# Kernel optimization log

Measured on AMD Instinct MI355X. Metric: run time of the kernel, lower is better.

The kernel has to match this reference:

```python
import jax, jax.numpy as jnp
import numpy as np

EPS = 1e-6


def _feature_map(x):
    # elu(x) + 1
    return jax.nn.elu(x) + 1.0


def _causal_dot(Qb, Kb, V):
    """Causal linear attention numerator for 3 stacked branches.
    Qb, Kb: [3, N, L, H, D]; V: [N, L, H, Dv] -> out [3, N, L, H, Dv].
    out[b,n,l,h,:] = sum_{s<=l} (Qb[b,n,l,h,:] . Kb[b,n,s,h,:]) V[n,s,h,:]
    computed with an O(L) recurrent scan over cumulative KV outer products.
    """
    Qs = jnp.moveaxis(Qb, 2, 0)  # [L, 3, N, H, D]
    Ks = jnp.moveaxis(Kb, 2, 0)  # [L, 3, N, H, D]
    Vs = jnp.moveaxis(V, 1, 0)   # [L, N, H, Dv]
    B, N, _, H, D = Qb.shape
    Dv = V.shape[-1]
    S0 = jnp.zeros((B, N, H, D, Dv), dtype=Qb.dtype)

    def step(S, inp):
        q, k, v = inp  # q,k: [3,N,H,D], v: [N,H,Dv]
        S = S + k[..., :, None] * v[None, :, :, None, :]
        o = jnp.einsum('bnhi,bnhij->bnhj', q, S)
        return S, o

    _, out = jax.lax.scan(step, S0, (Qs, Ks, Vs))  # out: [L,3,N,H,Dv]
    return jnp.moveaxis(out, 0, 2)  # [3,N,L,H,Dv]


def setup_inputs() -> dict:
    key = jax.random.key(0)
    ks = jax.random.split(key, 5)
    N, L, H, D = 4, 2048, 8, 128
    return {
        'queries': jax.random.normal(ks[0], (N, L, H, D), dtype=jnp.float32),
        'q2': jax.random.normal(ks[1], (N, L, H, D), dtype=jnp.float32),
        'keys': jax.random.normal(ks[2], (N, L, H, D), dtype=jnp.float32),
        'values': jax.random.normal(ks[3], (N, L, H, D), dtype=jnp.float32),
        'key_lengths': jnp.ones((N, L), dtype=jnp.float32),
        'omega': jax.random.normal(ks[4], (H, D, D), dtype=jnp.float32),
    }


def reference(queries, q2, keys, values, key_lengths, omega):
    N, L, H, D = queries.shape
    Q = _feature_map(queries)                       # [N,L,H,D]
    K = _feature_map(keys) * key_lengths[:, :, None, None]

    # Delta[n,l,h,i] = l/L for all n,h,i -> projection through omega reduces to
    # (l/L) * sum_i omega[h,i,j], same math as einsum('nlhi,hij->nlhj', Delta, omega).
    delta = (jnp.arange(L, dtype=queries.dtype) / L)        # [L]
    t = delta[:, None, None] * jnp.sum(omega, axis=1)[None]  # [L,H,D]
    sin_t, cos_t = jnp.sin(t), jnp.cos(t)
    s2, c2, sc = sin_t ** 2, cos_t ** 2, sin_t * cos_t       # [L,H,D] each

    # Q_term = sin(phi(q2))^2 * feature_map(queries)
    q2_proj = jnp.einsum('nlhi,hij->nlhj', q2, omega)
    Q_term = (jnp.sin(q2_proj) ** 2) * Q                     # [N,L,H,D]

    # Branch trig weights: Q gets [sin^2, cos^2, sin*cos], K gets [cos^2, sin^2, sin*cos]
    wq = jnp.stack([s2, c2, sc])[:, None]  # [3,1,L,H,D]
    wk = jnp.stack([c2, s2, sc])[:, None]
    Qb = Q_term[None] * wq                 # [3,N,L,H,D]
    Kb = K[None] * wk                      # [3,N,L,H,D]

    # Denominator terms Z_b = <Q_b[l], cumsum_{s<=l} K_b[s]>
    Kcum = jnp.cumsum(Kb, axis=2)
    Z = jnp.einsum('bnlhi,bnlhi->bnlh', Qb, Kcum)   # [3,N,L,H]

    Vb = _causal_dot(Qb, Kb, values)                # [3,N,L,H,D]

    numerator = Vb[0] + Vb[1] - 2.0 * Vb[2]
    denominator = Z[0] + Z[1] - 2.0 * Z[2] + EPS
    return numerator / denominator[:, :, :, None]
```

## Files before the change

kernel.cpp:

```cpp
#include <hip/hip_runtime.h>


typedef float f32x4 __attribute__((ext_vector_type(4)));
typedef short s16x8 __attribute__((ext_vector_type(8)));
typedef short s16x4 __attribute__((ext_vector_type(4)));
typedef unsigned short u16;

static constexpr int    Ln   = 2048;
static constexpr size_t NHLD = (size_t)32 * 2048 * 128;
static constexpr size_t KSB  = (size_t)32 * 16 * 128;

__device__ __forceinline__ float b2f(u16 s) {
  union { unsigned u; float f; } x; x.u = ((unsigned)s) << 16; return x.f;
}
__device__ __forceinline__ u16 f2b(float f) {
  union { float f; unsigned u; } x; x.f = f;
  unsigned r = x.u + 0x7fffu + ((x.u >> 16) & 1u);
  return (u16)(r >> 16);
}
__device__ __forceinline__ s16x8 pack8(f32x4 a, f32x4 b) {
  s16x8 r;
  r[0] = (short)f2b(a[0]); r[1] = (short)f2b(a[1]); r[2] = (short)f2b(a[2]); r[3] = (short)f2b(a[3]);
  r[4] = (short)f2b(b[0]); r[5] = (short)f2b(b[1]); r[6] = (short)f2b(b[2]); r[7] = (short)f2b(b[3]);
  return r;
}

__global__ __launch_bounds__(256) void k_omega(const float* __restrict__ om,
                                               u16* __restrict__ wt, float* __restrict__ osum) {
  __shared__ alignas(16) u16 T[128][136];
  int h = blockIdx.x, t = threadIdx.x;
  for (int idx = t; idx < 128 * 32; idx += 256) {
    int i = idx >> 5, cs = (idx & 31) << 2;
    f32x4 vv = *(const f32x4*)(om + ((size_t)(h * 128 + i)) * 128 + cs);
    T[i][cs + 0] = f2b(vv[0]); T[i][cs + 1] = f2b(vv[1]);
    T[i][cs + 2] = f2b(vv[2]); T[i][cs + 3] = f2b(vv[3]);
  }
  if (t < 128) {
    float acc = 0.f;
    for (int i = 0; i < 128; i++) acc += om[((size_t)(h * 128 + i)) * 128 + t];
    osum[h * 128 + t] = acc;
  }
  __syncthreads();
  {
    int j = t >> 1, lh = (t & 1) << 6;
    s16x8* dst = (s16x8*)(wt + ((size_t)(h * 128 + j)) * 128 + lh);
    for (int u = 0; u < 8; u++) {
      s16x8 pv;
#pragma unroll
      for (int e = 0; e < 8; e++) pv[e] = (short)T[lh + u * 8 + e][j];
      dst[u] = pv;
    }
  }
}

__global__ __launch_bounds__(256) void k_kvfeat(const float* __restrict__ kg, const float* __restrict__ vg,
                                                const float* __restrict__ klg, const float* __restrict__ osum,
                                                u16* __restrict__ kb3, u16* __restrict__ vt) {
  __shared__ alignas(16) u16 T[128][128];
  int bid = blockIdx.x, t = threadIdx.x;
  int c = bid & 15, h = (bid >> 4) & 7, n = bid >> 7;
  int l0 = c << 7, nh = (n << 3) + h;
  const float invL = 1.0f / 2048.0f;
  int gcol = t & 31, cs = gcol << 2;
  f32x4 osv = *(const f32x4*)(osum + h * 128 + cs);
#pragma unroll
  for (int it = 0; it < 16; it++) {
    int idx = (it << 8) + t;
    int rr = idx >> 5;
    int l = l0 + rr;
    size_t gb = (((size_t)(n * Ln + l) * 8 + h) << 7) + cs;
    f32x4 kv = *(const f32x4*)(kg + gb);
    f32x4 vv = *(const f32x4*)(vg + gb);
    float klv = klg[n * Ln + l];
    float tb = (float)l * invL;
    u16 r0[4], r1[4], r2[4];
#pragma unroll
    for (int e = 0; e < 4; e++) {
      float kf = (kv[e] > 0.f ? kv[e] + 1.f : __expf(kv[e])) * klv;
      float tt = tb * osv[e];
      float s, cc; __sincosf(tt, &s, &cc);
      r0[e] = f2b(kf * cc * cc);
      r1[e] = f2b(kf * s * s);
      r2[e] = f2b(kf * s * cc);
    }
    int gs = (gcol ^ (rr >> 3)) << 2;
    *(s16x4*)&T[rr][gs] = (s16x4){(short)f2b(vv[0]), (short)f2b(vv[1]),
                                  (short)f2b(vv[2]), (short)f2b(vv[3])};
    size_t nb = ((size_t)nh * Ln + l) * 128 + cs;
    *(s16x4*)(kb3 + nb)          = (s16x4){(short)r0[0], (short)r0[1], (short)r0[2], (short)r0[3]};
    *(s16x4*)(kb3 + NHLD + nb)   = (s16x4){(short)r1[0], (short)r1[1], (short)r1[2], (short)r1[3]};
    *(s16x4*)(kb3 + 2*NHLD + nb) = (s16x4){(short)r2[0], (short)r2[1], (short)r2[2], (short)r2[3]};
  }
  __syncthreads();
  {
    size_t bv = ((size_t)(nh * 16 + c)) << 14;
    for (int idx = t; idx < 2048; idx += 256) {
      int i = idx >> 4, o = idx & 15;
      int gp = (((i >> 2) ^ o) << 2) + (i & 3);
      s16x8 v1;
#pragma unroll
      for (int u = 0; u < 8; u++) v1[u] = (short)T[(o << 3) + u][gp];
      *(s16x8*)(vt + bv + (((size_t)i) << 7) + (o << 3)) = v1;
    }
  }
}

__global__ __launch_bounds__(512, 4) void p1a(const u16* __restrict__ vtg, const u16* __restrict__ kb3,
                                              u16* __restrict__ sct, float* __restrict__ ksum) {
  __shared__ alignas(16) u16 B[128][136];
  int bid = blockIdx.x, t = threadIdx.x;
  int c = bid & 15, h = (bid >> 4) & 7, n = (bid >> 7) & 3, b = bid >> 9;
  int l0 = c << 7, nh = (n << 3) + h, bnh = b * 32 + nh;
  int lane = t & 63, quad = lane >> 4, nl = lane & 15, w = t >> 6;
  const u16* kb = kb3 + (size_t)b * NHLD + ((size_t)nh * Ln + l0) * 128;
  for (int idx = t; idx < 2048; idx += 512) {
    int s = idx >> 4, io = idx & 15;
    s16x8 v = *(const s16x8*)(kb + (((size_t)s) << 7) + (io << 3));
    int cp = s ^ ((io & 7) << 3);
#pragma unroll
    for (int j = 0; j < 8; j++) B[(io << 3) + j][cp] = (u16)(short)v[j];
  }
  __syncthreads();
  f32x4 z4 = {0.f, 0.f, 0.f, 0.f};
  f32x4 acc[8];
#pragma unroll
  for (int i = 0; i < 8; i++) acc[i] = z4;
  int arow = (w << 4) + nl;
  size_t vbase = ((size_t)(nh * 16 + c)) << 14;
  for (int ks = 0; ks < 4; ks++) {
    int k0 = (ks << 5) + (quad << 3);
#pragma unroll
    for (int ct = 0; ct < 8; ct++) {
      int r = (ct << 4) + nl;
      int koff = k0 ^ (((r >> 3) & 7) << 3);
      s16x8 bv = *(const s16x8*)&B[r][koff];
      s16x8 av = *(const s16x8*)(vtg + vbase + (((size_t)arow) << 7) + k0);
      acc[ct] = __builtin_amdgcn_mfma_f32_16x16x32_bf16(av, bv, acc[ct], 0, 0, 0);
    }
  }
  if (t < 128) {
    float s = 0.f;
    int sw = ((t >> 3) & 7) << 3;
#pragma unroll 4
    for (int g = 0; g < 128; g += 8) {
      s16x8 v = *(const s16x8*)&B[t][g ^ sw];
#pragma unroll
      for (int e = 0; e < 8; e++) s += b2f((u16)v[e]);
    }
    ksum[(size_t)(bnh * 16 + c) * 128 + t] = s;
  }
  __syncthreads();
  {
    int lbase = (w << 4) + (quad << 2);
#pragma unroll
    for (int ct = 0; ct < 8; ct++) {
      int i = (ct << 4) + nl;
#pragma unroll
      for (int r = 0; r < 4; r++) B[lbase + r][i] = f2b(acc[ct][r]);
    }
  }
  __syncthreads();
  size_t sbase = ((size_t)(bnh * 16 + c)) << 14;
  for (int idx = t; idx < 2048; idx += 512) {
    int jr = idx >> 4, g = (idx & 15) << 3;
    *(s16x8*)(sct + sbase + ((size_t)jr << 7) + g) = *(const s16x8*)&B[jr][g];
  }
}

__global__ __launch_bounds__(256) void p1b(u16* __restrict__ sct, float* __restrict__ ksum) {
  int bid = blockIdx.x, t = threadIdx.x;
  if (bid < 768) {
    int tid = bid * 256 + t;
    int bnh = tid >> 11, rem = tid & 2047;
    size_t base = ((size_t)bnh << 18) + ((size_t)rem << 3);
    float acc[8] = {0.f, 0.f, 0.f, 0.f, 0.f, 0.f, 0.f, 0.f};
    for (int c = 0; c < 16; c++) {
      size_t a = base + ((size_t)c << 14);
      s16x8 v = *(const s16x8*)(sct + a);
      s16x8 o;
#pragma unroll
      for (int e = 0; e < 8; e++) { o[e] = (short)f2b(acc[e]); acc[e] += b2f((u16)v[e]); }
      *(s16x8*)(sct + a) = o;
    }
  } else {
    int m2 = (bid - 768) * 256 + t;
    int i = m2 & 127, bnh = m2 >> 7;
    size_t base = (size_t)bnh * 2048 + i;
    float acc = 0.f;
    for (int c = 0; c < 16; c++) {
      size_t a = base + (size_t)c * 128;
      float v = ksum[a];
      ksum[a] = acc;
      acc += v;
    }
  }
}

__global__ __launch_bounds__(256, 2) void k_qfeat(const float* __restrict__ q2g, const float* __restrict__ qg,
                                                  const u16* __restrict__ wt, const float* __restrict__ osum,
                                                  const float* __restrict__ kspre,
                                                  u16* __restrict__ qb3, float* __restrict__ zintg) {
  __shared__ alignas(16) u16 B[128][136];
  __shared__ float osb[128];
  int bid = blockIdx.x, t = threadIdx.x;
  int m = bid & 31, h = (bid >> 5) & 7, n = bid >> 8;
  int l0 = m << 6, c = m >> 1, nh = (n << 3) + h;
  if (t < 128) osb[t] = osum[h * 128 + t];
  for (int idx = t; idx < 2048; idx += 256) {
    int j = idx >> 4, cs = (idx & 15) << 3;
    *(s16x8*)&B[j][cs] = *(const s16x8*)(wt + ((size_t)(h * 128 + j)) * 128 + cs);
  }
  __syncthreads();
  int lane = t & 63, quad = lane >> 4, nl = lane & 15, w = t >> 6;
  f32x4 z4 = {0.f, 0.f, 0.f, 0.f};
  f32x4 acc[8];
#pragma unroll
  for (int i = 0; i < 8; i++) acc[i] = z4;
  int arow = l0 + (w << 4) + nl;
  for (int ks = 0; ks < 4; ks++) {
    int k0 = (ks << 5) + (quad << 3);
    const float* ap = q2g + (((size_t)(n * Ln + arow) * 8 + h) << 7) + k0;
    s16x8 av = pack8(*(const f32x4*)ap, *(const f32x4*)(ap + 4));
#pragma unroll
    for (int ct = 0; ct < 8; ct++) {
      s16x8 bv = *(const s16x8*)&B[(ct << 4) + nl][k0];
      acc[ct] = __builtin_amdgcn_mfma_f32_16x16x32_bf16(av, bv, acc[ct], 0, 0, 0);
    }
  }
  __syncthreads();
  {
    int lbase = (w << 4) + (quad << 2);
#pragma unroll
    for (int ct = 0; ct < 8; ct++) {
      int j = (ct << 4) + nl;
#pragma unroll
      for (int r = 0; r < 4; r++) {
        float sp = __sinf(acc[ct][r]);
        B[lbase + r][j] = f2b(sp * sp);
      }
    }
  }
  __syncthreads();
  const float invL = 1.0f / 2048.0f;
  for (int idx = t; idx < 1024; idx += 256) {
    int l = idx >> 4, j0 = (idx & 15) << 3, gl = l0 + l;
    s16x8 s2v = *(const s16x8*)&B[l][j0];
    const float* qp = qg + (((size_t)(n * Ln + gl) * 8 + h) << 7) + j0;
    f32x4 qa = *(const f32x4*)qp, qbv = *(const f32x4*)(qp + 4);
    size_t kbb = ((size_t)nh * 16 + c) * 128 + j0;
    f32x4 kp0a = *(const f32x4*)(kspre + kbb),           kp0b = *(const f32x4*)(kspre + kbb + 4);
    f32x4 kp1a = *(const f32x4*)(kspre + kbb + KSB),     kp1b = *(const f32x4*)(kspre + kbb + KSB + 4);
    f32x4 kp2a = *(const f32x4*)(kspre + kbb + 2 * KSB), kp2b = *(const f32x4*)(kspre + kbb + 2 * KSB + 4);
    s16x8 o0, o1, o2;
    float z = 0.f;
    float tb = (float)gl * invL;
#pragma unroll
    for (int e = 0; e < 8; e++) {
      float s2p = b2f((u16)s2v[e]);
      float qv = (e < 4) ? qa[e] : qbv[e - 4];
      float f = qv > 0.f ? qv + 1.f : __expf(qv);
      float Qt = s2p * f;
      float tt = tb * osb[j0 + e];
      float s, cc; __sincosf(tt, &s, &cc);
      float v0 = Qt * s * s, v1 = Qt * cc * cc, v2 = -2.f * Qt * s * cc;
      float k0v = (e < 4) ? kp0a[e] : kp0b[e - 4];
      float k1v = (e < 4) ? kp1a[e] : kp1b[e - 4];
      float k2v = (e < 4) ? kp2a[e] : kp2b[e - 4];
      z += v0 * k0v + v1 * k1v + v2 * k2v;
      o0[e] = (short)f2b(v0); o1[e] = (short)f2b(v1); o2[e] = (short)f2b(v2);
    }
    size_t base = ((size_t)nh * Ln + gl) * 128 + j0;
    *(s16x8*)(qb3 + base)            = o0;
    *(s16x8*)(qb3 + base + NHLD)     = o1;
    *(s16x8*)(qb3 + base + 2 * NHLD) = o2;
    z += __shfl_xor(z, 1); z += __shfl_xor(z, 2);
    z += __shfl_xor(z, 4); z += __shfl_xor(z, 8);
    if (nl == 0) zintg[(size_t)nh * Ln + gl] = z;
  }
}

__global__ __launch_bounds__(512, 4) void p3(const u16* __restrict__ qb3, const u16* __restrict__ kb3,
                                             const u16* __restrict__ vtg, const u16* __restrict__ sct,
                                             const float* __restrict__ zintg, float* __restrict__ outg) {
  __shared__ union {
    struct { alignas(16) u16 T0[128][128]; alignas(16) u16 T1[128][128]; } s;
    alignas(16) float O[128][132];
  } sm;
  int bid = blockIdx.x, t = threadIdx.x;
  int c = bid & 15, h = (bid >> 4) & 7, n = bid >> 7;
  int l0c = c << 7, nh = (n << 3) + h;
  int lane = t & 63, quad = lane >> 4, nl = lane & 15, w = t >> 6;
  f32x4 z4 = {0.f, 0.f, 0.f, 0.f};
  f32x4 accP[8], accO[8];
#pragma unroll
  for (int i = 0; i < 8; i++) { accP[i] = z4; accO[i] = z4; }
  int arow = l0c + (w << 4) + nl;
  for (int b = 0; b < 3; b++) {
    int bnh = b * 32 + nh;
    __syncthreads();
    for (int idx = t; idx < 2048; idx += 512) {
      int s = idx >> 4;
      int co = (((idx & 15) ^ (s & 7)) << 3);
      *(s16x8*)&sm.s.T0[s][co] = *(const s16x8*)(kb3 + (((size_t)bnh * Ln + l0c + s) << 7) + ((idx & 15) << 3));
    }
    size_t sbase = ((size_t)(bnh * 16 + c)) << 14;
    for (int idx = t; idx < 2048; idx += 512) {
      int j = idx >> 4;
      int co = (((idx & 15) ^ (j & 7)) << 3);
      *(s16x8*)&sm.s.T1[j][co] = *(const s16x8*)(sct + sbase + ((size_t)j << 7) + ((idx & 15) << 3));
    }
    s16x8 av[4];
#pragma unroll
    for (int ks = 0; ks < 4; ks++)
      av[ks] = *(const s16x8*)(qb3 + (((size_t)bnh * Ln + arow) << 7) + (ks << 5) + (quad << 3));
    __syncthreads();
    for (int ks = 0; ks < 4; ks++) {
      int k0 = (ks << 5) + (quad << 3);
#pragma unroll
      for (int ct = 0; ct < 8; ct++) {
        int r = (ct << 4) + nl;
        int koff = k0 ^ ((r & 7) << 3);
        s16x8 bv0 = *(const s16x8*)&sm.s.T0[r][koff];
        accP[ct] = __builtin_amdgcn_mfma_f32_16x16x32_bf16(av[ks], bv0, accP[ct], 0, 0, 0);
        s16x8 bv1 = *(const s16x8*)&sm.s.T1[r][koff];
        accO[ct] = __builtin_amdgcn_mfma_f32_16x16x32_bf16(av[ks], bv1, accO[ct], 0, 0, 0);
      }
    }
  }
  __syncthreads();
  float zP[4] = {0.f, 0.f, 0.f, 0.f};
  int lbase = (w << 4) + (quad << 2);
#pragma unroll
  for (int ct = 0; ct < 8; ct++) {
    int ss = (ct << 4) + nl;
#pragma unroll
    for (int r = 0; r < 4; r++) {
      int lr = lbase + r;
      float pv = (ss <= lr) ? accP[ct][r] : 0.f;
      zP[r] += pv;
      sm.s.T0[lr][ss ^ ((lr & 7) << 3)] = f2b(pv);
    }
  }
#pragma unroll
  for (int mteam = 1; mteam <= 8; mteam <<= 1) {
#pragma unroll
    for (int r = 0; r < 4; r++) zP[r] += __shfl_xor(zP[r], mteam);
  }
  size_t vbase = ((size_t)(nh * 16 + c)) << 14;
  for (int idx = t; idx < 2048; idx += 512) {
    int j = idx >> 4;
    int co = (((idx & 15) ^ (j & 7)) << 3);
    *(s16x8*)&sm.s.T1[j][co] = *(const s16x8*)(vtg + vbase + ((size_t)idx << 3));
  }
  float zf[4];
#pragma unroll
  for (int r = 0; r < 4; r++)
    zf[r] = zintg[(size_t)nh * Ln + l0c + lbase + r] + zP[r] + 1e-6f;
  __syncthreads();
  for (int ks = 0; ks < 4; ks++) {
    int k0 = (ks << 5) + (quad << 3);
    int rw = (w << 4) + nl;
    s16x8 pav = *(const s16x8*)&sm.s.T0[rw][k0 ^ ((rw & 7) << 3)];
#pragma unroll
    for (int ct = 0; ct < 8; ct++) {
      int r = (ct << 4) + nl;
      s16x8 vv = *(const s16x8*)&sm.s.T1[r][k0 ^ ((r & 7) << 3)];
      accO[ct] = __builtin_amdgcn_mfma_f32_16x16x32_bf16(pav, vv, accO[ct], 0, 0, 0);
    }
  }
  __syncthreads();
#pragma unroll
  for (int ct = 0; ct < 8; ct++) {
    int j = (ct << 4) + nl;
#pragma unroll
    for (int r = 0; r < 4; r++) sm.O[lbase + r][j] = accO[ct][r] / zf[r];
  }
  __syncthreads();
  for (int idx = t; idx < 4096; idx += 512) {
    int l = idx >> 5, g = (idx & 31) << 2;
    *(f32x4*)(outg + (((size_t)(n * Ln + l0c + l) * 8 + h) << 7) + g) = *(const f32x4*)&sm.O[l][g];
  }
}

extern "C" void kernel_launch(void* const* d_in, const int* in_sizes, int n_in,
                              void* d_out, int out_size, void* d_ws, size_t ws_size,
                              hipStream_t stream) {
  (void)in_sizes; (void)n_in; (void)out_size; (void)ws_size;
  const float* q   = (const float*)d_in[0];
  const float* q2  = (const float*)d_in[1];
  const float* kk  = (const float*)d_in[2];
  const float* vv  = (const float*)d_in[3];
  const float* kl  = (const float*)d_in[4];
  const float* om  = (const float*)d_in[5];
  float* out = (float*)d_out;

  u16* W     = (u16*)d_ws;
  u16* qb3   = W;
  u16* kb3   = W + 3 * NHLD;
  u16* vt    = W + 6 * NHLD;
  u16* sct   = W + 7 * NHLD;
  u16* wt    = W + 10 * NHLD;
  float* ks  = (float*)(W + 10 * NHLD + 131072);
  float* osm = ks + 196608;
  float* zin = osm + 1024;

  k_omega <<<8,    256, 0, stream>>>(om, wt, osm);
  k_kvfeat<<<512,  256, 0, stream>>>(kk, vv, kl, osm, kb3, vt);
  p1a     <<<1536, 512, 0, stream>>>(vt, kb3, sct, ks);
  p1b     <<<816,  256, 0, stream>>>(sct, ks);
  k_qfeat <<<1024, 256, 0, stream>>>(q2, q, wt, osm, ks, qb3, zin);
  p3      <<<512,  512, 0, stream>>>(qb3, kb3, vt, sct, zin, out);
}
```

Measured before the change: 270.2 us.

## Fuse K/V feature kernel with per-chunk KV outer-product kernel

Result: no change. 269.2 us (-0.4%).

```diff
diff --git a/kernel.cpp b/kernel.cpp
--- a/kernel.cpp
+++ b/kernel.cpp
@@ -53,10 +53,14 @@
   }
 }
 
-__global__ __launch_bounds__(256) void k_kvfeat(const float* __restrict__ kg, const float* __restrict__ vg,
-                                                const float* __restrict__ klg, const float* __restrict__ osum,
-                                                u16* __restrict__ kb3, u16* __restrict__ vt) {
-  __shared__ alignas(16) u16 T[128][128];
+__global__ __launch_bounds__(512) void k_kvs(const float* __restrict__ kg, const float* __restrict__ vg,
+                                             const float* __restrict__ klg, const float* __restrict__ osum,
+                                             u16* __restrict__ kb3, u16* __restrict__ vt,
+                                             u16* __restrict__ sct, float* __restrict__ ksum) {
+  __shared__ union {
+    alignas(16) u16 VT[128][128];
+    alignas(16) u16 KT[128][136];
+  } sm;
   int bid = blockIdx.x, t = threadIdx.x;
   int c = bid & 15, h = (bid >> 4) & 7, n = bid >> 7;
   int l0 = c << 7, nh = (n << 3) + h;
@@ -64,9 +68,8 @@
   int gcol = t & 31, cs = gcol << 2;
   f32x4 osv = *(const f32x4*)(osum + h * 128 + cs);
 #pragma unroll
-  for (int it = 0; it < 16; it++) {
-    int idx = (it << 8) + t;
-    int rr = idx >> 5;
+  for (int it = 0; it < 8; it++) {
+    int rr = (it << 4) + (t >> 5);
     int l = l0 + rr;
     size_t gb = (((size_t)(n * Ln + l) * 8 + h) << 7) + cs;
     f32x4 kv = *(const f32x4*)(kg + gb);
@@ -84,86 +87,80 @@
       r2[e] = f2b(kf * s * cc);
     }
     int gs = (gcol ^ (rr >> 3)) << 2;
-    *(s16x4*)&T[rr][gs] = (s16x4){(short)f2b(vv[0]), (short)f2b(vv[1]),
-                                  (short)f2b(vv[2]), (short)f2b(vv[3])};
+    *(s16x4*)&sm.VT[rr][gs] = (s16x4){(short)f2b(vv[0]), (short)f2b(vv[1]),
+                                      (short)f2b(vv[2]), (short)f2b(vv[3])};
     size_t nb = ((size_t)nh * Ln + l) * 128 + cs;
     *(s16x4*)(kb3 + nb)          = (s16x4){(short)r0[0], (short)r0[1], (short)r0[2], (short)r0[3]};
     *(s16x4*)(kb3 + NHLD + nb)   = (s16x4){(short)r1[0], (short)r1[1], (short)r1[2], (short)r1[3]};
     *(s16x4*)(kb3 + 2*NHLD + nb) = (s16x4){(short)r2[0], (short)r2[1], (short)r2[2], (short)r2[3]};
   }
   __syncthreads();
-  {
-    size_t bv = ((size_t)(nh * 16 + c)) << 14;
-    for (int idx = t; idx < 2048; idx += 256) {
-      int i = idx >> 4, o = idx & 15;
-      int gp = (((i >> 2) ^ o) << 2) + (i & 3);
-      s16x8 v1;
-#pragma unroll
-      for (int u = 0; u < 8; u++) v1[u] = (short)T[(o << 3) + u][gp];
-      *(s16x8*)(vt + bv + (((size_t)i) << 7) + (o << 3)) = v1;
-    }
-  }
-}
-
-__global__ __launch_bounds__(512, 4) void p1a(const u16* __restrict__ vtg, const u16* __restrict__ kb3,
-                                              u16* __restrict__ sct, float* __restrict__ ksum) {
-  __shared__ alignas(16) u16 B[128][136];
-  int bid = blockIdx.x, t = threadIdx.x;
-  int c = bid & 15, h = (bid >> 4) & 7, n = (bid >> 7) & 3, b = bid >> 9;
-  int l0 = c << 7, nh = (n << 3) + h, bnh = b * 32 + nh;
+  size_t bv = ((size_t)(nh * 16 + c)) << 14;
+  for (int idx = t; idx < 2048; idx += 512) {
+    int i = idx >> 4, o = idx & 15;
+    int gp = (((i >> 2) ^ o) << 2) + (i & 3);
+    s16x8 v1;
+#pragma unroll
+    for (int u = 0; u < 8; u++) v1[u] = (short)sm.VT[(o << 3) + u][gp];
+    *(s16x8*)(vt + bv + (((size_t)i) << 7) + (o << 3)) = v1;
+  }
   int lane = t & 63, quad = lane >> 4, nl = lane & 15, w = t >> 6;
-  const u16* kb = kb3 + (size_t)b * NHLD + ((size_t)nh * Ln + l0) * 128;
-  for (int idx = t; idx < 2048; idx += 512) {
-    int s = idx >> 4, io = idx & 15;
-    s16x8 v = *(const s16x8*)(kb + (((size_t)s) << 7) + (io << 3));
-    int cp = s ^ ((io & 7) << 3);
-#pragma unroll
-    for (int j = 0; j < 8; j++) B[(io << 3) + j][cp] = (u16)(short)v[j];
-  }
-  __syncthreads();
-  f32x4 z4 = {0.f, 0.f, 0.f, 0.f};
-  f32x4 acc[8];
-#pragma unroll
-  for (int i = 0; i < 8; i++) acc[i] = z4;
   int arow = (w << 4) + nl;
-  size_t vbase = ((size_t)(nh * 16 + c)) << 14;
-  for (int ks = 0; ks < 4; ks++) {
-    int k0 = (ks << 5) + (quad << 3);
-#pragma unroll
-    for (int ct = 0; ct < 8; ct++) {
-      int r = (ct << 4) + nl;
-      int koff = k0 ^ (((r >> 3) & 7) << 3);
-      s16x8 bv = *(const s16x8*)&B[r][koff];
-      s16x8 av = *(const s16x8*)(vtg + vbase + (((size_t)arow) << 7) + k0);
-      acc[ct] = __builtin_amdgcn_mfma_f32_16x16x32_bf16(av, bv, acc[ct], 0, 0, 0);
-    }
-  }
-  if (t < 128) {
-    float s = 0.f;
-    int sw = ((t >> 3) & 7) << 3;
+  const u16* vchunk = vt + bv;
+  for (int b = 0; b < 3; b++) {
+    int bnh = b * 32 + nh;
+    const u16* kb = kb3 + (size_t)b * NHLD + ((size_t)nh * Ln + l0) * 128;
+    __syncthreads();
+    for (int idx = t; idx < 2048; idx += 512) {
+      int s = idx >> 4, io = idx & 15;
+      s16x8 v = *(const s16x8*)(kb + (((size_t)s) << 7) + (io << 3));
+      int cp = s ^ ((io & 7) << 3);
+#pragma unroll
+      for (int j = 0; j < 8; j++) sm.KT[(io << 3) + j][cp] = (u16)(short)v[j];
+    }
+    __syncthreads();
+    f32x4 z4 = {0.f, 0.f, 0.f, 0.f};
+    f32x4 acc[8];
+#pragma unroll
+    for (int i = 0; i < 8; i++) acc[i] = z4;
+    for (int ks = 0; ks < 4; ks++) {
+      int k0 = (ks << 5) + (quad << 3);
+      s16x8 av = *(const s16x8*)(vchunk + (((size_t)arow) << 7) + k0);
+#pragma unroll
+      for (int ct = 0; ct < 8; ct++) {
+        int r = (ct << 4) + nl;
+        int koff = k0 ^ (((r >> 3) & 7) << 3);
+        s16x8 bvv = *(const s16x8*)&sm.KT[r][koff];
+        acc[ct] = __builtin_amdgcn_mfma_f32_16x16x32_bf16(av, bvv, acc[ct], 0, 0, 0);
+      }
+    }
+    if (t < 128) {
+      float s = 0.f;
+      int sw = ((t >> 3) & 7) << 3;
 #pragma unroll 4
-    for (int g = 0; g < 128; g += 8) {
-      s16x8 v = *(const s16x8*)&B[t][g ^ sw];
-#pragma unroll
-      for (int e = 0; e < 8; e++) s += b2f((u16)v[e]);
-    }
-    ksum[(size_t)(bnh * 16 + c) * 128 + t] = s;
-  }
-  __syncthreads();
-  {
-    int lbase = (w << 4) + (quad << 2);
-#pragma unroll
-    for (int ct = 0; ct < 8; ct++) {
-      int i = (ct << 4) + nl;
-#pragma unroll
-      for (int r = 0; r < 4; r++) B[lbase + r][i] = f2b(acc[ct][r]);
-    }
-  }
-  __syncthreads();
-  size_t sbase = ((size_t)(bnh * 16 + c)) << 14;
-  for (int idx = t; idx < 2048; idx += 512) {
-    int jr = idx >> 4, g = (idx & 15) << 3;
-    *(s16x8*)(sct + sbase + ((size_t)jr << 7) + g) = *(const s16x8*)&B[jr][g];
+      for (int g = 0; g < 128; g += 8) {
+        s16x8 v = *(const s16x8*)&sm.KT[t][g ^ sw];
+#pragma unroll
+        for (int e = 0; e < 8; e++) s += b2f((u16)v[e]);
+      }
+      ksum[(size_t)(bnh * 16 + c) * 128 + t] = s;
+    }
+    __syncthreads();
+    {
+      int lbase = (w << 4) + (quad << 2);
+#pragma unroll
+      for (int ct = 0; ct < 8; ct++) {
+        int i = (ct << 4) + nl;
+#pragma unroll
+        for (int r = 0; r < 4; r++) sm.KT[lbase + r][i] = f2b(acc[ct][r]);
+      }
+    }
+    __syncthreads();
+    size_t sbase = ((size_t)(bnh * 16 + c)) << 14;
+    for (int idx = t; idx < 2048; idx += 512) {
+      int jr = idx >> 4, g = (idx & 15) << 3;
+      *(s16x8*)(sct + sbase + ((size_t)jr << 7) + g) = *(const s16x8*)&sm.KT[jr][g];
+    }
   }
 }
 
@@ -405,8 +402,7 @@
   float* zin = osm + 1024;
 
   k_omega <<<8,    256, 0, stream>>>(om, wt, osm);
-  k_kvfeat<<<512,  256, 0, stream>>>(kk, vv, kl, osm, kb3, vt);
-  p1a     <<<1536, 512, 0, stream>>>(vt, kb3, sct, ks);
+  k_kvs   <<<512,  512, 0, stream>>>(kk, vv, kl, osm, kb3, vt, sct, ks);
   p1b     <<<816,  256, 0, stream>>>(sct, ks);
   k_qfeat <<<1024, 256, 0, stream>>>(q2, q, wt, osm, ks, qb3, zin);
   p3      <<<512,  512, 0, stream>>>(qb3, kb3, vt, sct, zin, out);
```
